# Optimization experiments

Hardware: AMD Instinct MI355X
Metric: run time of the kernel (lower is better)

The kernel has to match this reference:

```python
import math
import jax, jax.numpy as jnp
import numpy as np

N_FFT = 1024
HOP = 320
WIN = 800
SR = 32000
N_MELS = 128
FMIN = 0.0
FMAX = SR / 2.0
NUM_BINS = N_FFT // 2 + 1  # 513
PREEMPH = 0.97


def _hann_window(n):
    # torch.hann_window(n, periodic=False): 0.5 - 0.5*cos(2*pi*i/(n-1))
    i = np.arange(n, dtype=np.float64)
    return (0.5 - 0.5 * np.cos(2.0 * np.pi * i / (n - 1))).astype(np.float32)


def _fourier_basis():
    offset = (N_FFT - WIN) // 2
    win_full = np.zeros(N_FFT, dtype=np.float64)
    win_full[offset:offset + WIN] = _hann_window(WIN)
    n = np.arange(N_FFT, dtype=np.float64)[None, :]
    k = np.arange(NUM_BINS, dtype=np.float64)[:, None]
    ang = 2.0 * np.pi * k * (n / float(N_FFT))
    cos_k = np.cos(ang) * win_full
    sin_k = -np.sin(ang) * win_full
    return np.concatenate([cos_k, sin_k], axis=0).astype(np.float32)  # [2*513, 1024]


def _kaldi_mel_banks():
    # torchaudio.compliance.kaldi.get_mel_banks with vtln_warp_factor=1.0
    num_fft_bins = N_FFT // 2
    fft_bin_width = SR / float(N_FFT)
    mel = lambda f: 1127.0 * np.log(1.0 + f / 700.0)
    mel_low, mel_high = mel(FMIN), mel(FMAX)
    delta = (mel_high - mel_low) / (N_MELS + 1)
    left = mel_low + np.arange(N_MELS, dtype=np.float64) * delta  # [M]
    right = left + 2.0 * delta
    freqs = fft_bin_width * np.arange(num_fft_bins, dtype=np.float64)
    m = mel(freqs)[None, :]  # [1, 512]
    up = (m - left[:, None]) / delta
    down = (right[:, None] - m) / delta
    bank = np.maximum(0.0, np.minimum(up, down))  # [128, 512]
    bank = np.pad(bank, ((0, 0), (0, 1)))  # pad one zero column -> [128, 513]
    return bank.astype(np.float32)


def setup_inputs() -> dict:
    key = jax.random.key(0)
    x = jax.random.normal(key, (32, 320000), dtype=jnp.float32)
    return {
        "x": x,
        "fourier_basis": jnp.asarray(_fourier_basis()),
        "mel_basis": jnp.asarray(_kaldi_mel_banks()),
    }


def reference(x, fourier_basis, mel_basis):
    # preemphasis: conv1d with kernel [-0.97, 1.0] (cross-correlation)
    y = x[:, 1:] - PREEMPH * x[:, :-1]  # [B, T-1]
    # center pad by n_fft//2
    pad = N_FFT // 2
    y = jnp.pad(y, ((0, 0), (pad, pad)))
    Tp = y.shape[1]
    frames = (Tp - N_FFT) // HOP + 1
    # frame extraction: [B, frames, n_fft]
    idx = jnp.arange(frames)[:, None] * HOP + jnp.arange(N_FFT)[None, :]
    f = y[:, idx]
    # explicit DFT via dense matmul: [B, 2*num_bins, frames]
    spec = jnp.einsum('btn,cn->bct', f, fourier_basis)
    real = spec[:, :NUM_BINS, :]
    imag = spec[:, NUM_BINS:, :]
    power = real * real + imag * imag  # [B, num_bins, frames]
    mel = jnp.einsum('mf,bft->bmt', mel_basis, power)
    log_mel = (jnp.log(mel + 1e-05) + 4.5) / 5.0
    return log_mel
```

## Files before the change

### kernel.cpp

```cpp
#include <hip/hip_runtime.h>
#include <math.h>

typedef _Float16 half8 __attribute__((ext_vector_type(8)));
typedef float f32x4 __attribute__((ext_vector_type(4)));

constexpr int kNFFT    = 1024;
constexpr int kHop     = 320;
constexpr int kMels    = 128;
constexpr int kFrames  = 1000;
constexpr int kBatch   = 32;
constexpr int kXLen    = 320000;
constexpr int kYLen    = kXLen - 1;
constexpr int kYPad    = 328704;
constexpr int kYOff    = 512;
constexpr float kPre   = 0.97f;
constexpr int kPStride = 544;
constexpr int kKsLo    = 3;
constexpr int kKsHi    = 28;

constexpr size_t kYLvl     = (size_t)kBatch * kYPad;
constexpr size_t kFragLvl  = 64ull * 32 * 64 * 8;
constexpr size_t kFragOff  = 2 * kYLvl;
constexpr size_t kMelFrOff = kFragOff + 2 * kFragLvl;
constexpr size_t kMelFrSz  = 8ull * 17 * 64 * 8;
constexpr size_t kPowOff   = kMelFrOff + kMelFrSz;

constexpr int kYJobBlks   = (kYPad / 8 + 255) / 256;
constexpr int kYJobTotal  = kYJobBlks * kBatch;
constexpr int kFragBlks   = 131072 / 256;
constexpr int kMelBlks    = (8 * 17 * 64) / 256;
constexpr int kPrepGrid   = kYJobTotal + kFragBlks + kMelBlks;

__global__ void prep_all(const float* __restrict__ x, const float* __restrict__ basis,
                         const float* __restrict__ melb, _Float16* __restrict__ ws) {
    _Float16* ypad  = ws;
    _Float16* fr    = ws + kFragOff;
    _Float16* melfr = ws + kMelFrOff;
    const int bid = blockIdx.x;
    const int tid = threadIdx.x;

    if (bid < kYJobTotal) {
        int b = bid / kYJobBlks;
        int blk = bid - b * kYJobBlks;
        int e0 = (blk * 256 + tid) * 8;
        if (e0 >= kYPad) return;
        const float* xb = x + (size_t)b * kXLen;
        int yi = e0 - kYOff;
        float v[8];
        if (yi >= 0 && yi <= kXLen - 9) {
            float4 A = *(const float4*)(xb + yi);
            float4 B = *(const float4*)(xb + yi + 4);
            float C = xb[yi + 8];
            v[0] = A.y - kPre * A.x;  v[1] = A.z - kPre * A.y;
            v[2] = A.w - kPre * A.z;  v[3] = B.x - kPre * A.w;
            v[4] = B.y - kPre * B.x;  v[5] = B.z - kPre * B.y;
            v[6] = B.w - kPre * B.z;  v[7] = C   - kPre * B.w;
        } else {
            #pragma unroll
            for (int j = 0; j < 8; ++j) {
                int g = yi + j;
                v[j] = (g >= 0 && g < kYLen) ? xb[g + 1] - kPre * xb[g] : 0.0f;
            }
        }
        half8 hv, mv;
        #pragma unroll
        for (int j = 0; j < 8; ++j) {
            _Float16 h = (_Float16)v[j];
            hv[j] = h;
            mv[j] = (_Float16)(v[j] - (float)h);
        }
        size_t idx = (size_t)b * kYPad + e0;
        *(half8*)(ypad + idx) = hv;
        *(half8*)(ypad + idx + kYLvl) = mv;
    } else if (bid < kYJobTotal + kFragBlks) {
        int id = (bid - kYJobTotal) * 256 + tid;
        int L  = id & 63;
        int ks = (id >> 6) & 31;
        int g  = id >> 11;
        int r  = 16 * g + (L & 15);
        int orig = (r <= 512) ? r : r + 1;
        const float* src = basis + (size_t)orig * kNFFT + 32 * ks + (L >> 4) * 8;
        _Float16* dst = fr + (size_t)id * 8;
        #pragma unroll
        for (int j = 0; j < 8; ++j) {
            float a = src[j];
            _Float16 h = (_Float16)a;
            _Float16 m = (_Float16)(a - (float)h);
            dst[j] = h;
            dst[j + kFragLvl] = m;
        }
    } else {
        int id = (bid - kYJobTotal - kFragBlks) * 256 + tid;
        if (id >= 8 * 17 * 64) return;
        int f = id / 1088;
        int rem = id - f * 1088;
        int ks = rem >> 6;
        int L = rem & 63;
        int m = 16 * f + (L & 15);
        int kb = 32 * ks + (L >> 4) * 8;
        _Float16* dst = melfr + (size_t)id * 8;
        #pragma unroll
        for (int j = 0; j < 8; ++j) {
            int k = kb + j;
            dst[j] = (k < 513) ? (_Float16)melb[(size_t)m * 513 + k] : (_Float16)0.0f;
        }
    }
}

__global__ __launch_bounds__(512, 2)
void stft_power(const _Float16* __restrict__ frags,
                const _Float16* __restrict__ ypad,
                _Float16* __restrict__ pw) {
    __shared__ __align__(16) _Float16 ash[2][16 * 512];
    const int tid  = threadIdx.x;
    const int w    = tid >> 6;
    const int lane = tid & 63;
    const int quad = lane >> 4;
    const int l16  = lane & 15;
    const int nt = blockIdx.x, g = blockIdx.y, b = blockIdx.z;
    const int t0 = nt * 512 + w * 64;
    const _Float16* yb0 = ypad + (size_t)b * kYPad;
    const _Float16* yb1 = yb0 + kYLvl;

    f32x4 acc[8][4] = {};

    auto stageA = [&](int ks, int pbuf) {
        #pragma unroll
        for (int c = 0; c < 2; ++c) {
            int slot = w + 8 * c;
            int f = slot & 7, lv = slot >> 3;
            int Gf = (f < 4) ? (4 * g + f) : (32 + 4 * g + (f - 4));
            const _Float16* gp = frags + (size_t)lv * kFragLvl
                               + ((size_t)(Gf * 32 + ks) * 64 + lane) * 8;
            __builtin_amdgcn_global_load_lds(
                (const __attribute__((address_space(1))) void*)gp,
                (__attribute__((address_space(3))) void*)&ash[pbuf][slot * 512],
                16, 0, 0);
        }
    };
    auto loadB = [&](int ks, half8* bh, half8* bm) {
        #pragma unroll
        for (int nf = 0; nf < 4; ++nf) {
            int off = (t0 + nf * 16 + l16) * kHop + ks * 32 + quad * 8;
            bh[nf] = *(const half8*)(yb0 + off);
            bm[nf] = *(const half8*)(yb1 + off);
        }
    };
    auto compute = [&](int pbuf, half8* bh, half8* bm) {
        #pragma unroll
        for (int f = 0; f < 8; ++f) {
            half8 afh = *(const half8*)&ash[pbuf][f * 512 + lane * 8];
            half8 afm = *(const half8*)&ash[pbuf][(8 + f) * 512 + lane * 8];
            #pragma unroll
            for (int nf = 0; nf < 4; ++nf) {
                f32x4 a = acc[f][nf];
                a = __builtin_amdgcn_mfma_f32_16x16x32_f16(afh, bh[nf], a, 0, 0, 0);
                a = __builtin_amdgcn_mfma_f32_16x16x32_f16(afm, bh[nf], a, 0, 0, 0);
                a = __builtin_amdgcn_mfma_f32_16x16x32_f16(afh, bm[nf], a, 0, 0, 0);
                acc[f][nf] = a;
            }
        }
    };

    half8 bhA[4], bmA[4], bhB[4], bmB[4];
    stageA(kKsLo, 0);
    loadB(kKsLo, bhA, bmA);
    for (int kss = 0; kss < 13; ++kss) {
        int ks = kKsLo + 2 * kss;
        __syncthreads();
        stageA(ks + 1, 1);
        loadB(ks + 1, bhB, bmB);
        compute(0, bhA, bmA);
        __syncthreads();
        if (ks + 2 <= kKsHi) {
            stageA(ks + 2, 0);
            loadB(ks + 2, bhA, bmA);
        }
        compute(1, bhB, bmB);
    }

    #pragma unroll
    for (int mf = 0; mf < 4; ++mf) {
        int b0 = 64 * g + 16 * mf + 4 * quad;
        #pragma unroll
        for (int nf = 0; nf < 4; ++nf) {
            int t = t0 + nf * 16 + l16;
            size_t row = ((size_t)((b << 10) + t)) * kPStride;
            struct alignas(8) h4 { _Float16 v[4]; } pp;
            #pragma unroll
            for (int rr = 0; rr < 4; ++rr) {
                float pA = acc[mf][nf][rr];
                float pB = acc[4 + mf][nf][rr];
                float p2 = pA * pA + pB * pB;
                if (g == 0 && mf == 0 && quad == 0 && rr == 0) {
                    p2 = pA * pA;
                    pw[row + 512] = (_Float16)(pB * pB);
                }
                pp.v[rr] = (_Float16)p2;
            }
            *(decltype(pp)*)&pw[row + b0] = pp;
        }
    }
}

__global__ __launch_bounds__(256)
void mel_mfma(const _Float16* __restrict__ melfr, const _Float16* __restrict__ pw,
              float* __restrict__ out) {
    const int tid  = threadIdx.x;
    const int w    = tid >> 6;
    const int lane = tid & 63;
    const int quad = lane >> 4;
    const int l16  = lane & 15;
    const int nt = blockIdx.x, b = blockIdx.y;
    const int t0 = nt * 128 + w * 32;

    f32x4 acc[8][2] = {};
    for (int ks = 0; ks < 17; ++ks) {
        half8 bp[2];
        #pragma unroll
        for (int nf = 0; nf < 2; ++nf) {
            int t = t0 + nf * 16 + l16;
            bp[nf] = *(const half8*)(pw + ((size_t)((b << 10) + t)) * kPStride
                                     + 32 * ks + quad * 8);
        }
        #pragma unroll
        for (int f = 0; f < 8; ++f) {
            half8 af = *(const half8*)(melfr + ((size_t)(f * 17 + ks) * 64 + lane) * 8);
            #pragma unroll
            for (int nf = 0; nf < 2; ++nf)
                acc[f][nf] = __builtin_amdgcn_mfma_f32_16x16x32_f16(af, bp[nf], acc[f][nf], 0, 0, 0);
        }
    }
    #pragma unroll
    for (int f = 0; f < 8; ++f) {
        #pragma unroll
        for (int nf = 0; nf < 2; ++nf) {
            int t = t0 + nf * 16 + l16;
            if (t < kFrames) {
                #pragma unroll
                for (int r = 0; r < 4; ++r) {
                    int m = 16 * f + 4 * quad + r;
                    out[((size_t)(b * kMels + m)) * kFrames + t] =
                        (__logf(acc[f][nf][r] + 1e-5f) + 4.5f) * 0.2f;
                }
            }
        }
    }
}

extern "C" void kernel_launch(void* const* d_in, const int* in_sizes, int n_in,
                              void* d_out, int out_size, void* d_ws, size_t ws_size,
                              hipStream_t stream) {
    const float* x     = (const float*)d_in[0];
    const float* basis = (const float*)d_in[1];
    const float* melb  = (const float*)d_in[2];
    float* out = (float*)d_out;

    _Float16* ws    = (_Float16*)d_ws;
    _Float16* frags = ws + kFragOff;
    _Float16* melfr = ws + kMelFrOff;
    _Float16* pw    = ws + kPowOff;

    prep_all<<<dim3(kPrepGrid), 256, 0, stream>>>(x, basis, melb, ws);
    stft_power<<<dim3(2, 8, kBatch), 512, 0, stream>>>(frags, ws, pw);
    mel_mfma<<<dim3(8, kBatch), 256, 0, stream>>>(melfr, pw, out);
}
```

Baseline: 265.1 us.

## Load STFT basis fragments directly to registers and halve block size

Drops the LDS double-buffered staging of the Fourier basis fragments, so each wave now loads its A fragments straight from global memory into registers with per-fragment pointers advanced each k-step. The __syncthreads barriers go away. Blocks shrink to 256 threads covering 256 frames, and the grid doubles along x. This removes barrier and LDS traffic, but every wave now fetches the full A set on its own, which puts more load on L2/global, and the software prefetch that overlapped loads with MFMA is lost.

```diff
diff --git a/kernel.cpp b/kernel.cpp
--- a/kernel.cpp
+++ b/kernel.cpp
@@ -107,76 +107,68 @@
     }
 }
 
-__global__ __launch_bounds__(512, 2)
+__global__ __launch_bounds__(256, 2)
 void stft_power(const _Float16* __restrict__ frags,
                 const _Float16* __restrict__ ypad,
                 _Float16* __restrict__ pw) {
-    __shared__ __align__(16) _Float16 ash[2][16 * 512];
     const int tid  = threadIdx.x;
     const int w    = tid >> 6;
     const int lane = tid & 63;
     const int quad = lane >> 4;
     const int l16  = lane & 15;
     const int nt = blockIdx.x, g = blockIdx.y, b = blockIdx.z;
-    const int t0 = nt * 512 + w * 64;
+    const int t0 = nt * 256 + w * 64;
     const _Float16* yb0 = ypad + (size_t)b * kYPad;
     const _Float16* yb1 = yb0 + kYLvl;
 
     f32x4 acc[8][4] = {};
 
-    auto stageA = [&](int ks, int pbuf) {
-        #pragma unroll
-        for (int c = 0; c < 2; ++c) {
-            int slot = w + 8 * c;
-            int f = slot & 7, lv = slot >> 3;
+    const _Float16* abase[2][8];
+    #pragma unroll
+    for (int lv = 0; lv < 2; ++lv)
+        #pragma unroll
+        for (int f = 0; f < 8; ++f) {
             int Gf = (f < 4) ? (4 * g + f) : (32 + 4 * g + (f - 4));
-            const _Float16* gp = frags + (size_t)lv * kFragLvl
-                               + ((size_t)(Gf * 32 + ks) * 64 + lane) * 8;
-            __builtin_amdgcn_global_load_lds(
-                (const __attribute__((address_space(1))) void*)gp,
-                (__attribute__((address_space(3))) void*)&ash[pbuf][slot * 512],
-                16, 0, 0);
-        }
-    };
-    auto loadB = [&](int ks, half8* bh, half8* bm) {
+            abase[lv][f] = frags + (size_t)lv * kFragLvl
+                         + ((size_t)(Gf * 32 + kKsLo) * 64 + lane) * 8;
+        }
+    const _Float16* bbase0[4];
+    const _Float16* bbase1[4];
+    #pragma unroll
+    for (int nf = 0; nf < 4; ++nf) {
+        int off = (t0 + nf * 16 + l16) * kHop + kKsLo * 32 + quad * 8;
+        bbase0[nf] = yb0 + off;
+        bbase1[nf] = yb1 + off;
+    }
+
+    for (int ks = kKsLo; ks <= kKsHi; ++ks) {
+        half8 ah[8], am[8];
+        #pragma unroll
+        for (int f = 0; f < 8; ++f) {
+            ah[f] = *(const half8*)abase[0][f];
+            am[f] = *(const half8*)abase[1][f];
+            abase[0][f] += 512;
+            abase[1][f] += 512;
+        }
+        half8 bh[4], bm[4];
         #pragma unroll
         for (int nf = 0; nf < 4; ++nf) {
-            int off = (t0 + nf * 16 + l16) * kHop + ks * 32 + quad * 8;
-            bh[nf] = *(const half8*)(yb0 + off);
-            bm[nf] = *(const half8*)(yb1 + off);
-        }
-    };
-    auto compute = [&](int pbuf, half8* bh, half8* bm) {
-        #pragma unroll
-        for (int f = 0; f < 8; ++f) {
-            half8 afh = *(const half8*)&ash[pbuf][f * 512 + lane * 8];
-            half8 afm = *(const half8*)&ash[pbuf][(8 + f) * 512 + lane * 8];
+            bh[nf] = *(const half8*)bbase0[nf];
+            bm[nf] = *(const half8*)bbase1[nf];
+            bbase0[nf] += 32;
+            bbase1[nf] += 32;
+        }
+        #pragma unroll
+        for (int f = 0; f < 8; ++f) {
             #pragma unroll
             for (int nf = 0; nf < 4; ++nf) {
                 f32x4 a = acc[f][nf];
-                a = __builtin_amdgcn_mfma_f32_16x16x32_f16(afh, bh[nf], a, 0, 0, 0);
-                a = __builtin_amdgcn_mfma_f32_16x16x32_f16(afm, bh[nf], a, 0, 0, 0);
-                a = __builtin_amdgcn_mfma_f32_16x16x32_f16(afh, bm[nf], a, 0, 0, 0);
+                a = __builtin_amdgcn_mfma_f32_16x16x32_f16(ah[f], bh[nf], a, 0, 0, 0);
+                a = __builtin_amdgcn_mfma_f32_16x16x32_f16(am[f], bh[nf], a, 0, 0, 0);
+                a = __builtin_amdgcn_mfma_f32_16x16x32_f16(ah[f], bm[nf], a, 0, 0, 0);
                 acc[f][nf] = a;
             }
         }
-    };
-
-    half8 bhA[4], bmA[4], bhB[4], bmB[4];
-    stageA(kKsLo, 0);
-    loadB(kKsLo, bhA, bmA);
-    for (int kss = 0; kss < 13; ++kss) {
-        int ks = kKsLo + 2 * kss;
-        __syncthreads();
-        stageA(ks + 1, 1);
-        loadB(ks + 1, bhB, bmB);
-        compute(0, bhA, bmA);
-        __syncthreads();
-        if (ks + 2 <= kKsHi) {
-            stageA(ks + 2, 0);
-            loadB(ks + 2, bhA, bmA);
-        }
-        compute(1, bhB, bmB);
     }
 
     #pragma unroll
@@ -262,6 +254,6 @@
     _Float16* pw    = ws + kPowOff;
 
     prep_all<<<dim3(kPrepGrid), 256, 0, stream>>>(x, basis, melb, ws);
-    stft_power<<<dim3(2, 8, kBatch), 512, 0, stream>>>(frags, ws, pw);
+    stft_power<<<dim3(4, 8, kBatch), 256, 0, stream>>>(frags, ws, pw);
     mel_mfma<<<dim3(8, kBatch), 256, 0, stream>>>(melfr, pw, out);
 }
```

After: 266.8 us. No clear change (+0.6%).
